# Performance work log

Hardware: AMD Instinct MI355X
Metric: run time of the kernel (lower is better)

The kernel has to match this reference:

```python
import jax, jax.numpy as jnp
import numpy as np

# module-level constants from the source
TIME = 50
SCALE = 1.0
OFFSET = 1.0
THRESH_ENC = 0.5
THRESH_PLUS = 0.03
LEAK = 1.0

BATCH, FEAT = 256, 4096


def setup_inputs() -> dict:
    key = jax.random.key(0)
    x = jax.random.normal(key, (BATCH, 1, FEAT), dtype=jnp.float32)
    return {"x": x}


def reference(x):
    """Faithful jax version of SNN._encode: 50-step integrate-fire-reset
    spike encoding with adaptive threshold, fused into a single lax.scan.
    Returns spikes of shape [B, 1, F, TIME] (float 0/1; torch used uint8)."""
    current = x * SCALE + OFFSET                      # injected current, constant per step
    v0 = jnp.zeros_like(x)                            # membrane voltage
    t0 = jnp.full_like(x, THRESH_ENC)                 # adaptive threshold

    def step(carry, _):
        v, th = carry
        v = v + current                               # integrate
        s = (v >= th).astype(x.dtype)                 # fire
        v = jnp.where(s > 0, 0.0, v) * LEAK           # reset + leak (leak=1.0)
        th = th + s * THRESH_PLUS                     # threshold adaptation
        return (v, th), s

    _, spikes = jax.lax.scan(step, (v0, t0), None, length=TIME)  # [TIME, B, 1, F]
    return jnp.moveaxis(spikes, 0, -1)                # [B, 1, F, TIME]
```

## Files before the change

### kernel.cpp

```cpp
#include <hip/hip_runtime.h>
#include <stdint.h>


#define TIME 50
#define BLOCK 256
#define EPB 512
#define REGION (EPB * TIME)
#define NQUADS (REGION / 4)
#define ITERS (NQUADS / BLOCK)

__global__ __launch_bounds__(BLOCK) void snn_encode_kernel(
    const float* __restrict__ x, float* __restrict__ out, int n_elems) {
    __shared__ unsigned long long sb[EPB];

    const int tid = threadIdx.x;
    const int base = blockIdx.x * EPB;

    #pragma unroll
    for (int h = 0; h < 2; ++h) {
        const int le = tid + h * BLOCK;
        const int elem = base + le;
        unsigned long long bits = 0ull;
        if (elem < n_elems) {
            const float cur = x[elem] * 1.0f + 1.0f;
            float v = 0.0f;
            float th = 0.5f;
            #pragma unroll
            for (int t = 0; t < TIME; ++t) {
                v += cur;
                if (v >= th) {
                    v = 0.0f;
                    th += 0.03f;
                    bits |= (1ull << t);
                }
            }
        }
        sb[le] = bits;
    }
    __syncthreads();

    float* dst = out + (size_t)blockIdx.x * REGION;
    #pragma unroll 5
    for (int it = 0; it < ITERS; ++it) {
        const int j = (it * BLOCK + tid) * 4;
        float vals[4];
        #pragma unroll
        for (int i = 0; i < 4; ++i) {
            const int jj = j + i;
            const int e = jj / TIME;
            const int t = jj - e * TIME;
            vals[i] = (float)((sb[e] >> t) & 1ull);
        }
        *reinterpret_cast<float4*>(dst + j) =
            make_float4(vals[0], vals[1], vals[2], vals[3]);
    }
}

extern "C" void kernel_launch(void* const* d_in, const int* in_sizes, int n_in,
                              void* d_out, int out_size, void* d_ws, size_t ws_size,
                              hipStream_t stream) {
    const float* x = (const float*)d_in[0];
    float* out = (float*)d_out;
    const int n = in_sizes[0];
    const int blocks = (n + EPB - 1) / EPB;
    snn_encode_kernel<<<blocks, BLOCK, 0, stream>>>(x, out, n);
}
```

Measured before the change: 37.07 us.

## Replace shared-memory transpose with warp shuffles and per-warp float2 stores

```diff
diff --git a/kernel.cpp b/kernel.cpp
--- a/kernel.cpp
+++ b/kernel.cpp
@@ -4,30 +4,35 @@
 
 #define TIME 50
 #define BLOCK 256
-#define EPB 512
-#define REGION (EPB * TIME)
-#define NQUADS (REGION / 4)
-#define ITERS (NQUADS / BLOCK)
+#define WARP 64
+#define CHUNKS 4
+#define EPW (CHUNKS * WARP)
+#define EPB ((BLOCK / WARP) * EPW)
+
+typedef float f32x2 __attribute__((ext_vector_type(2)));
 
 __global__ __launch_bounds__(BLOCK) void snn_encode_kernel(
     const float* __restrict__ x, float* __restrict__ out, int n_elems) {
-    __shared__ unsigned long long sb[EPB];
+    const int lane = threadIdx.x & (WARP - 1);
+    const int wid = threadIdx.x >> 6;
+    const int wbase = blockIdx.x * EPB + wid * EPW;
 
-    const int tid = threadIdx.x;
-    const int base = blockIdx.x * EPB;
+    float cur[CHUNKS];
+    #pragma unroll
+    for (int c = 0; c < CHUNKS; ++c) {
+        const int elem = wbase + c * WARP + lane;
+        cur[c] = (elem < n_elems) ? (x[elem] * 1.0f + 1.0f) : 0.0f;
+    }
 
     #pragma unroll
-    for (int h = 0; h < 2; ++h) {
-        const int le = tid + h * BLOCK;
-        const int elem = base + le;
+    for (int c = 0; c < CHUNKS; ++c) {
         unsigned long long bits = 0ull;
-        if (elem < n_elems) {
-            const float cur = x[elem] * 1.0f + 1.0f;
+        {
             float v = 0.0f;
             float th = 0.5f;
             #pragma unroll
             for (int t = 0; t < TIME; ++t) {
-                v += cur;
+                v += cur[c];
                 if (v >= th) {
                     v = 0.0f;
                     th += 0.03f;
@@ -35,24 +40,19 @@
                 }
             }
         }
-        sb[le] = bits;
-    }
-    __syncthreads();
 
-    float* dst = out + (size_t)blockIdx.x * REGION;
-    #pragma unroll 5
-    for (int it = 0; it < ITERS; ++it) {
-        const int j = (it * BLOCK + tid) * 4;
-        float vals[4];
-        #pragma unroll
-        for (int i = 0; i < 4; ++i) {
-            const int jj = j + i;
-            const int e = jj / TIME;
-            const int t = jj - e * TIME;
-            vals[i] = (float)((sb[e] >> t) & 1ull);
+        float* cdst = out + (size_t)(wbase + c * WARP) * TIME;
+        #pragma unroll 5
+        for (int it = 0; it < 25; ++it) {
+            const int k = it * WARP + lane;
+            const int e = k / 25;
+            const int t2 = (k - e * 25) * 2;
+            const unsigned long long b = __shfl(bits, e, WARP);
+            f32x2 vals;
+            vals.x = (float)((b >> t2) & 1ull);
+            vals.y = (float)((b >> (t2 + 1)) & 1ull);
+            *reinterpret_cast<f32x2*>(cdst + k * 2) = vals;
         }
-        *reinterpret_cast<float4*>(dst + j) =
-            make_float4(vals[0], vals[1], vals[2], vals[3]);
     }
 }
 
```

Measured after the change: 37.44 us. No clear change (+1.0%).
